# Kernel tuning notes

Hardware: AMD Instinct MI355X
Metric: run time of the kernel (lower is better)

## Reference

```python
import jax, jax.numpy as jnp
import numpy as np

T, HW, C = 64, 24, 1024
MID = 256
WIN = 2  # 'video' forward_type -> 2x2 windows


def setup_inputs() -> dict:
    key = jax.random.key(0)
    k1, k2, k3, k4, k5 = jax.random.split(key, 5)
    return {
        "image_features": jax.random.normal(k1, (T, HW * HW, C), dtype=jnp.float32),
        "Wq": jax.random.normal(k2, (C, MID), dtype=jnp.float32) * 0.02,
        "bq": jax.random.normal(k3, (MID,), dtype=jnp.float32) * 0.02,
        "Wk": jax.random.normal(k4, (C, MID), dtype=jnp.float32) * 0.02,
        "bk": jax.random.normal(k5, (MID,), dtype=jnp.float32) * 0.02,
    }


def reference(image_features, Wq, bq, Wk, bk):
    # forward_type == 'video': 2x2 windowed attention over pooled patches
    t, n, c = image_features.shape
    H = W = int(np.sqrt(n))
    h2, w2 = H // WIN, W // WIN
    # [T, H, W, C] -> [T, h2, 2, w2, 2, C] -> [T, h2, w2, 2, 2, C] -> [T, P, 4, C]
    x = image_features.reshape(t, h2, WIN, w2, WIN, c)
    windows = x.transpose(0, 1, 3, 2, 4, 5).reshape(t, h2 * w2, WIN * WIN, c)
    # avg_pool2d(2,2) == mean over each 2x2 window
    pooled = windows.mean(axis=2)  # [T, P, C]
    q = pooled @ Wq + bq           # [T, P, MID]
    k = windows @ Wk + bk          # [T, P, 4, MID]
    scale = 1.0 / jnp.sqrt(jnp.float32(MID))
    attn = jnp.einsum("tpd,tpwd->tpw", q, k) * scale  # [T, P, 4]
    attn = jnp.nan_to_num(attn)
    attn = jax.nn.softmax(attn, axis=-1)
    attn_feat = jnp.einsum("tpw,tpwc->tpc", attn, windows)  # softmax-weighted value avg
    # query dim has size 1, so .mean(1) in torch is identity here
    return pooled + attn_feat  # [T, P, C]; new_image_size = (h2, w2) is static
```

## Files before the change

kernel.cpp:

```cpp
#include <hip/hip_runtime.h>

#define T_ 64
#define P_ 144
#define NPAIR 9216
#define C_ 1024
#define MID_ 256

typedef __attribute__((ext_vector_type(4))) float f32x4;
typedef __attribute__((ext_vector_type(8))) __bf16 bf16x8;
typedef __attribute__((ext_vector_type(4))) __bf16 bf16x4;

__device__ __forceinline__ void async_copy16(const void* g, void* l) {
  __builtin_amdgcn_global_load_lds(
      (const __attribute__((address_space(1))) unsigned int*)g,
      (__attribute__((address_space(3))) unsigned int*)l, 16, 0, 0);
}

__device__ __forceinline__ void mfma_tile(const __bf16* As, const __bf16* Bs,
                                          int wm, int wn, int quad, int lr,
                                          f32x4 acc[4][4]) {
  bf16x8 a[4], b[4];
  const bf16x8* Ap = (const bf16x8*)As;
  const bf16x8* Bp = (const bf16x8*)Bs;
#pragma unroll
  for (int i = 0; i < 4; ++i) {
    a[i] = Ap[(wm * 64 + i * 16 + lr) * 4 + quad];
    b[i] = Bp[(wn * 64 + i * 16 + lr) * 4 + quad];
  }
#pragma unroll
  for (int mi = 0; mi < 4; ++mi)
#pragma unroll
    for (int ni = 0; ni < 4; ++ni)
      acc[mi][ni] = __builtin_amdgcn_mfma_f32_16x16x32_bf16(
          a[mi], b[ni], acc[mi][ni], 0, 0, 0);
}

__global__ __launch_bounds__(256) void prep_kernel(
    const float* __restrict__ img, const float* __restrict__ Wq,
    const float* __restrict__ bq, const float* __restrict__ Wk,
    __bf16* __restrict__ poolb, __bf16* __restrict__ H,
    float* __restrict__ kb) {
  __shared__ __align__(16) __bf16 As[128 * 32];
  __shared__ __align__(16) __bf16 Bs[128 * 32];
  const int bid = blockIdx.x;
  const int tid = threadIdx.x;
  if (bid < NPAIR) {
    const int t = bid / P_;
    const int p = bid - t * P_;
    const int wy = p / 12, wx = p - wy * 12;
    const int c = tid * 4;
    const float* base = img + ((size_t)t * 576 + 48 * wy + 2 * wx) * C_;
    f32x4 s = *(const f32x4*)(base + c);
    s += *(const f32x4*)(base + (size_t)1 * C_ + c);
    s += *(const f32x4*)(base + (size_t)24 * C_ + c);
    s += *(const f32x4*)(base + (size_t)25 * C_ + c);
    s *= 0.25f;
    bf16x4 pv;
#pragma unroll
    for (int j = 0; j < 4; ++j) pv[j] = (__bf16)s[j];
    *(bf16x4*)(poolb + (size_t)bid * C_ + c) = pv;
  } else if (bid < NPAIR + 64) {
    const int b = bid - NPAIR;
    const int mt = b >> 3, nt = b & 7;
    const int lane = tid & 63;
    const int wv = tid >> 6;
    const int quad = lane >> 4, lr = lane & 15;
    const int wm = wv >> 1, wn = wv & 1;
    const int r0 = tid >> 2, p0 = tid & 3;
    const float* ga0 = Wk + (size_t)(mt * 128 + r0) * MID_ + p0 * 8;
    const float* ga1 = ga0 + (size_t)64 * MID_;
    const float* gb0 = Wq + (size_t)(nt * 128 + r0) * MID_ + p0 * 8;
    const float* gb1 = gb0 + (size_t)64 * MID_;
    f32x4 acc[4][4] = {};
    for (int it = 0; it < 8; ++it) {
      const f32x4 a0 = *(const f32x4*)ga0, a1 = *(const f32x4*)(ga0 + 4);
      const f32x4 a2 = *(const f32x4*)ga1, a3 = *(const f32x4*)(ga1 + 4);
      const f32x4 b0 = *(const f32x4*)gb0, b1 = *(const f32x4*)(gb0 + 4);
      const f32x4 b2 = *(const f32x4*)gb1, b3 = *(const f32x4*)(gb1 + 4);
      ga0 += 32; ga1 += 32; gb0 += 32; gb1 += 32;
      bf16x8 ca0, ca1, cb0, cb1;
#pragma unroll
      for (int j = 0; j < 4; ++j) {
        ca0[j] = (__bf16)a0[j]; ca0[4 + j] = (__bf16)a1[j];
        ca1[j] = (__bf16)a2[j]; ca1[4 + j] = (__bf16)a3[j];
        cb0[j] = (__bf16)b0[j]; cb0[4 + j] = (__bf16)b1[j];
        cb1[j] = (__bf16)b2[j]; cb1[4 + j] = (__bf16)b3[j];
      }
      *(bf16x8*)(As + (size_t)tid * 8) = ca0;
      *(bf16x8*)(As + (size_t)(tid + 256) * 8) = ca1;
      *(bf16x8*)(Bs + (size_t)tid * 8) = cb0;
      *(bf16x8*)(Bs + (size_t)(tid + 256) * 8) = cb1;
      __syncthreads();
      mfma_tile(As, Bs, wm, wn, quad, lr, acc);
      __syncthreads();
    }
    const int colb = nt * 128 + wn * 64;
    const int rowb = mt * 128 + wm * 64 + quad * 4;
#pragma unroll
    for (int ni = 0; ni < 4; ++ni) {
      const int col = colb + ni * 16 + lr;
#pragma unroll
      for (int mi = 0; mi < 4; ++mi) {
        const int row = rowb + mi * 16;
#pragma unroll
        for (int r = 0; r < 4; ++r)
          H[(size_t)(row + r) * C_ + col] = (__bf16)acc[mi][ni][r];
      }
    }
  } else {
    __shared__ float bqs[256];
    bqs[tid] = bq[tid];
    __syncthreads();
    const int n = (bid - (NPAIR + 64)) * 256 + tid;
    const float* row = Wk + (size_t)n * MID_;
    float s = 0.f;
#pragma unroll 4
    for (int j = 0; j < 256; ++j) s += row[j] * bqs[j];
    kb[n] = s;
  }
}

__global__ __launch_bounds__(256) void gemm_u_kernel(
    const __bf16* __restrict__ A, const __bf16* __restrict__ Bt,
    const float* __restrict__ bias, __bf16* __restrict__ C) {
  __shared__ __align__(16) __bf16 As[128 * 32];
  __shared__ __align__(16) __bf16 Bs[128 * 32];
  const int bid = blockIdx.x;
  const int mt = bid >> 3, nt = bid & 7;
  const int tid = threadIdx.x;
  const int lane = tid & 63;
  const int wv = tid >> 6;
  const int quad = lane >> 4, lr = lane & 15;
  const int wm = wv >> 1, wn = wv & 1;

  const int r0 = tid >> 2, p0 = tid & 3;
  const int wvb = (tid & ~63) * 16;
  const __bf16* ga0 = A + ((size_t)mt * 128 + r0) * (size_t)C_ + p0 * 8;
  const __bf16* ga1 = ga0 + (size_t)64 * C_;
  const __bf16* gb0 = Bt + ((size_t)nt * 128 + r0) * (size_t)C_ + p0 * 8;
  const __bf16* gb1 = gb0 + (size_t)64 * C_;
  char* AsB0 = (char*)As + wvb;
  char* AsB1 = (char*)As + 4096 + wvb;
  char* BsB0 = (char*)Bs + wvb;
  char* BsB1 = (char*)Bs + 4096 + wvb;

  f32x4 acc[4][4] = {};

  for (int it = 0; it < 32; ++it) {
    async_copy16(ga0, AsB0);
    async_copy16(ga1, AsB1);
    async_copy16(gb0, BsB0);
    async_copy16(gb1, BsB1);
    ga0 += 32; ga1 += 32; gb0 += 32; gb1 += 32;
    __syncthreads();
    mfma_tile(As, Bs, wm, wn, quad, lr, acc);
    __syncthreads();
  }

  const int colb = nt * 128 + wn * 64;
  const int rowb = mt * 128 + wm * 64 + quad * 4;
#pragma unroll
  for (int ni = 0; ni < 4; ++ni) {
    const int col = colb + ni * 16 + lr;
    const float bv = bias[col];
#pragma unroll
    for (int mi = 0; mi < 4; ++mi) {
      const int row = rowb + mi * 16;
#pragma unroll
      for (int r = 0; r < 4; ++r)
        C[(size_t)(row + r) * C_ + col] = (__bf16)(acc[mi][ni][r] + bv);
    }
  }
}

__global__ void attn_out_kernel(const __bf16* __restrict__ U,
                                const float* __restrict__ img,
                                float* __restrict__ out) {
  const int pair = blockIdx.x;
  const int tid = threadIdx.x;
  const int wv = tid >> 6, lane = tid & 63;
  __shared__ float red[4][4];

  const int t = pair / P_;
  const int pp = pair - t * P_;
  const int wy = pp / 12, wx = pp - wy * 12;
  const float* base = img + ((size_t)t * 576 + 48 * wy + 2 * wx) * C_;
  const int c = tid * 4;
  f32x4 v0 = *(const f32x4*)(base + c);
  f32x4 v1 = *(const f32x4*)(base + (size_t)1 * C_ + c);
  f32x4 v2 = *(const f32x4*)(base + (size_t)24 * C_ + c);
  f32x4 v3 = *(const f32x4*)(base + (size_t)25 * C_ + c);
  const bf16x4 ub = *(const bf16x4*)(U + (size_t)pair * C_ + c);
  f32x4 u4;
#pragma unroll
  for (int j = 0; j < 4; ++j) u4[j] = (float)ub[j];

  float pd[4];
  pd[0] = u4[0] * v0[0] + u4[1] * v0[1] + u4[2] * v0[2] + u4[3] * v0[3];
  pd[1] = u4[0] * v1[0] + u4[1] * v1[1] + u4[2] * v1[2] + u4[3] * v1[3];
  pd[2] = u4[0] * v2[0] + u4[1] * v2[1] + u4[2] * v2[2] + u4[3] * v2[3];
  pd[3] = u4[0] * v3[0] + u4[1] * v3[1] + u4[2] * v3[2] + u4[3] * v3[3];

#pragma unroll
  for (int w = 0; w < 4; ++w) {
    float p = pd[w];
    p += __shfl_down(p, 32);
    p += __shfl_down(p, 16);
    p += __shfl_down(p, 8);
    p += __shfl_down(p, 4);
    p += __shfl_down(p, 2);
    p += __shfl_down(p, 1);
    if (lane == 0) red[w][wv] = p;
  }
  __syncthreads();
  float lg[4];
  float mx = -1e30f;
#pragma unroll
  for (int w = 0; w < 4; ++w) {
    lg[w] = (red[w][0] + red[w][1] + red[w][2] + red[w][3]) * 0.0625f;
    mx = fmaxf(mx, lg[w]);
  }
  float att[4];
  float ssum = 0.f;
#pragma unroll
  for (int w = 0; w < 4; ++w) {
    att[w] = __expf(lg[w] - mx);
    ssum += att[w];
  }
  const float inv = 1.f / ssum;
  const float a0 = att[0] * inv, a1 = att[1] * inv;
  const float a2 = att[2] * inv, a3 = att[3] * inv;

  f32x4 o = (v0 + v1 + v2 + v3) * 0.25f;
  o += a0 * v0 + a1 * v1 + a2 * v2 + a3 * v3;
  *(f32x4*)(out + (size_t)pair * C_ + c) = o;
}

extern "C" void kernel_launch(void* const* d_in, const int* in_sizes, int n_in,
                              void* d_out, int out_size, void* d_ws,
                              size_t ws_size, hipStream_t stream) {
  const float* img = (const float*)d_in[0];
  const float* Wq = (const float*)d_in[1];
  const float* bq = (const float*)d_in[2];
  const float* Wk = (const float*)d_in[3];
  const float* bk = (const float*)d_in[4];
  (void)bk;
  float* out = (float*)d_out;

  char* ws = (char*)d_ws;
  __bf16* poolb = (__bf16*)ws;
  __bf16* H = (__bf16*)(ws + 18874368);
  float* kb = (float*)(ws + 20971520);
  __bf16* U = (__bf16*)(ws + 20975616);

  prep_kernel<<<NPAIR + 68, 256, 0, stream>>>(img, Wq, bq, Wk, poolb, H, kb);
  gemm_u_kernel<<<576, 256, 0, stream>>>(poolb, H, kb, U);
  attn_out_kernel<<<NPAIR, 256, 0, stream>>>(U, img, out);
}
```

Baseline: 297.3 us.

## Fuse pooling, U GEMM and attention output into one per-16-window kernel

```diff
diff --git a/kernel.cpp b/kernel.cpp
--- a/kernel.cpp
+++ b/kernel.cpp
@@ -6,15 +6,13 @@
 #define C_ 1024
 #define MID_ 256
 
+#define MP 16
+#define PST 1032
+#define UST 1028
+
 typedef __attribute__((ext_vector_type(4))) float f32x4;
 typedef __attribute__((ext_vector_type(8))) __bf16 bf16x8;
 typedef __attribute__((ext_vector_type(4))) __bf16 bf16x4;
-
-__device__ __forceinline__ void async_copy16(const void* g, void* l) {
-  __builtin_amdgcn_global_load_lds(
-      (const __attribute__((address_space(1))) unsigned int*)g,
-      (__attribute__((address_space(3))) unsigned int*)l, 16, 0, 0);
-}
 
 __device__ __forceinline__ void mfma_tile(const __bf16* As, const __bf16* Bs,
                                           int wm, int wn, int quad, int lr,
@@ -36,32 +34,15 @@
 }
 
 __global__ __launch_bounds__(256) void prep_kernel(
-    const float* __restrict__ img, const float* __restrict__ Wq,
-    const float* __restrict__ bq, const float* __restrict__ Wk,
-    __bf16* __restrict__ poolb, __bf16* __restrict__ H,
+    const float* __restrict__ Wq, const float* __restrict__ bq,
+    const float* __restrict__ Wk, __bf16* __restrict__ H,
     float* __restrict__ kb) {
   __shared__ __align__(16) __bf16 As[128 * 32];
   __shared__ __align__(16) __bf16 Bs[128 * 32];
   const int bid = blockIdx.x;
   const int tid = threadIdx.x;
-  if (bid < NPAIR) {
-    const int t = bid / P_;
-    const int p = bid - t * P_;
-    const int wy = p / 12, wx = p - wy * 12;
-    const int c = tid * 4;
-    const float* base = img + ((size_t)t * 576 + 48 * wy + 2 * wx) * C_;
-    f32x4 s = *(const f32x4*)(base + c);
-    s += *(const f32x4*)(base + (size_t)1 * C_ + c);
-    s += *(const f32x4*)(base + (size_t)24 * C_ + c);
-    s += *(const f32x4*)(base + (size_t)25 * C_ + c);
-    s *= 0.25f;
-    bf16x4 pv;
-#pragma unroll
-    for (int j = 0; j < 4; ++j) pv[j] = (__bf16)s[j];
-    *(bf16x4*)(poolb + (size_t)bid * C_ + c) = pv;
-  } else if (bid < NPAIR + 64) {
-    const int b = bid - NPAIR;
-    const int mt = b >> 3, nt = b & 7;
+  if (bid < 64) {
+    const int mt = bid >> 3, nt = bid & 7;
     const int lane = tid & 63;
     const int wv = tid >> 6;
     const int quad = lane >> 4, lr = lane & 15;
@@ -111,7 +92,7 @@
     __shared__ float bqs[256];
     bqs[tid] = bq[tid];
     __syncthreads();
-    const int n = (bid - (NPAIR + 64)) * 256 + tid;
+    const int n = (bid - 64) * 256 + tid;
     const float* row = Wk + (size_t)n * MID_;
     float s = 0.f;
 #pragma unroll 4
@@ -120,120 +101,113 @@
   }
 }
 
-__global__ __launch_bounds__(256) void gemm_u_kernel(
-    const __bf16* __restrict__ A, const __bf16* __restrict__ Bt,
-    const float* __restrict__ bias, __bf16* __restrict__ C) {
-  __shared__ __align__(16) __bf16 As[128 * 32];
-  __shared__ __align__(16) __bf16 Bs[128 * 32];
+__global__ __launch_bounds__(512, 4) void fused_kernel(
+    const __bf16* __restrict__ H, const float* __restrict__ kb,
+    const float* __restrict__ img, float* __restrict__ out) {
+  __shared__ __align__(16) char ubuf[MP * UST * 4];
+  __shared__ float kbs[C_];
+  __bf16* pool_s = (__bf16*)ubuf;
+  float* u_s = (float*)ubuf;
+
+  const int tid = threadIdx.x;
   const int bid = blockIdx.x;
-  const int mt = bid >> 3, nt = bid & 7;
-  const int tid = threadIdx.x;
   const int lane = tid & 63;
   const int wv = tid >> 6;
   const int quad = lane >> 4, lr = lane & 15;
-  const int wm = wv >> 1, wn = wv & 1;
-
-  const int r0 = tid >> 2, p0 = tid & 3;
-  const int wvb = (tid & ~63) * 16;
-  const __bf16* ga0 = A + ((size_t)mt * 128 + r0) * (size_t)C_ + p0 * 8;
-  const __bf16* ga1 = ga0 + (size_t)64 * C_;
-  const __bf16* gb0 = Bt + ((size_t)nt * 128 + r0) * (size_t)C_ + p0 * 8;
-  const __bf16* gb1 = gb0 + (size_t)64 * C_;
-  char* AsB0 = (char*)As + wvb;
-  char* AsB1 = (char*)As + 4096 + wvb;
-  char* BsB0 = (char*)Bs + wvb;
-  char* BsB1 = (char*)Bs + 4096 + wvb;
-
-  f32x4 acc[4][4] = {};
-
-  for (int it = 0; it < 32; ++it) {
-    async_copy16(ga0, AsB0);
-    async_copy16(ga1, AsB1);
-    async_copy16(gb0, BsB0);
-    async_copy16(gb1, BsB1);
-    ga0 += 32; ga1 += 32; gb0 += 32; gb1 += 32;
-    __syncthreads();
-    mfma_tile(As, Bs, wm, wn, quad, lr, acc);
-    __syncthreads();
-  }
-
-  const int colb = nt * 128 + wn * 64;
-  const int rowb = mt * 128 + wm * 64 + quad * 4;
-#pragma unroll
-  for (int ni = 0; ni < 4; ++ni) {
-    const int col = colb + ni * 16 + lr;
-    const float bv = bias[col];
-#pragma unroll
-    for (int mi = 0; mi < 4; ++mi) {
-      const int row = rowb + mi * 16;
-#pragma unroll
-      for (int r = 0; r < 4; ++r)
-        C[(size_t)(row + r) * C_ + col] = (__bf16)(acc[mi][ni][r] + bv);
-    }
-  }
-}
-
-__global__ void attn_out_kernel(const __bf16* __restrict__ U,
-                                const float* __restrict__ img,
-                                float* __restrict__ out) {
-  const int pair = blockIdx.x;
-  const int tid = threadIdx.x;
-  const int wv = tid >> 6, lane = tid & 63;
-  __shared__ float red[4][4];
-
-  const int t = pair / P_;
-  const int pp = pair - t * P_;
+
+  const int p = tid >> 5;
+  const int lp = tid & 31;
+  const int gp = bid * MP + p;
+  const int t = gp / P_;
+  const int pp = gp - t * P_;
   const int wy = pp / 12, wx = pp - wy * 12;
   const float* base = img + ((size_t)t * 576 + 48 * wy + 2 * wx) * C_;
-  const int c = tid * 4;
-  f32x4 v0 = *(const f32x4*)(base + c);
-  f32x4 v1 = *(const f32x4*)(base + (size_t)1 * C_ + c);
-  f32x4 v2 = *(const f32x4*)(base + (size_t)24 * C_ + c);
-  f32x4 v3 = *(const f32x4*)(base + (size_t)25 * C_ + c);
-  const bf16x4 ub = *(const bf16x4*)(U + (size_t)pair * C_ + c);
-  f32x4 u4;
-#pragma unroll
-  for (int j = 0; j < 4; ++j) u4[j] = (float)ub[j];
-
-  float pd[4];
-  pd[0] = u4[0] * v0[0] + u4[1] * v0[1] + u4[2] * v0[2] + u4[3] * v0[3];
-  pd[1] = u4[0] * v1[0] + u4[1] * v1[1] + u4[2] * v1[2] + u4[3] * v1[3];
-  pd[2] = u4[0] * v2[0] + u4[1] * v2[1] + u4[2] * v2[2] + u4[3] * v2[3];
-  pd[3] = u4[0] * v3[0] + u4[1] * v3[1] + u4[2] * v3[2] + u4[3] * v3[3];
-
-#pragma unroll
-  for (int w = 0; w < 4; ++w) {
-    float p = pd[w];
-    p += __shfl_down(p, 32);
-    p += __shfl_down(p, 16);
-    p += __shfl_down(p, 8);
-    p += __shfl_down(p, 4);
-    p += __shfl_down(p, 2);
-    p += __shfl_down(p, 1);
-    if (lane == 0) red[w][wv] = p;
-  }
+
+#pragma unroll
+  for (int j = 0; j < 8; ++j) {
+    const int c = lp * 4 + j * 128;
+    f32x4 s = *(const f32x4*)(base + c);
+    s += *(const f32x4*)(base + C_ + c);
+    s += *(const f32x4*)(base + 24 * C_ + c);
+    s += *(const f32x4*)(base + 25 * C_ + c);
+    s *= 0.25f;
+    bf16x4 pv;
+#pragma unroll
+    for (int q = 0; q < 4; ++q) pv[q] = (__bf16)s[q];
+    *(bf16x4*)(pool_s + p * PST + c) = pv;
+  }
+  if (tid < 256) *(f32x4*)(kbs + tid * 4) = *(const f32x4*)(kb + tid * 4);
   __syncthreads();
-  float lg[4];
-  float mx = -1e30f;
-#pragma unroll
-  for (int w = 0; w < 4; ++w) {
-    lg[w] = (red[w][0] + red[w][1] + red[w][2] + red[w][3]) * 0.0625f;
-    mx = fmaxf(mx, lg[w]);
-  }
-  float att[4];
-  float ssum = 0.f;
-#pragma unroll
-  for (int w = 0; w < 4; ++w) {
-    att[w] = __expf(lg[w] - mx);
-    ssum += att[w];
-  }
-  const float inv = 1.f / ssum;
-  const float a0 = att[0] * inv, a1 = att[1] * inv;
-  const float a2 = att[2] * inv, a3 = att[3] * inv;
-
-  f32x4 o = (v0 + v1 + v2 + v3) * 0.25f;
-  o += a0 * v0 + a1 * v1 + a2 * v2 + a3 * v3;
-  *(f32x4*)(out + (size_t)pair * C_ + c) = o;
+
+  f32x4 acc[8] = {};
+  const __bf16* ap = pool_s + lr * PST + quad * 8;
+  const __bf16* hp[8];
+#pragma unroll
+  for (int j = 0; j < 8; ++j)
+    hp[j] = H + (size_t)(wv * 128 + j * 16 + lr) * C_ + quad * 8;
+  for (int it = 0; it < 32; ++it) {
+    const bf16x8 a = *(const bf16x8*)(ap + it * 32);
+    bf16x8 b[8];
+#pragma unroll
+    for (int j = 0; j < 8; ++j) b[j] = *(const bf16x8*)(hp[j] + it * 32);
+#pragma unroll
+    for (int j = 0; j < 8; ++j)
+      acc[j] = __builtin_amdgcn_mfma_f32_16x16x32_bf16(a, b[j], acc[j], 0, 0, 0);
+  }
+  __syncthreads();
+
+#pragma unroll
+  for (int j = 0; j < 8; ++j) {
+    const int col = wv * 128 + j * 16 + lr;
+    const float kv = kbs[col];
+#pragma unroll
+    for (int r = 0; r < 4; ++r)
+      u_s[(quad * 4 + r) * UST + col] = acc[j][r] + kv;
+  }
+  __syncthreads();
+
+  float pd0 = 0.f, pd1 = 0.f, pd2 = 0.f, pd3 = 0.f;
+  for (int j = 0; j < 8; ++j) {
+    const int c = lp * 4 + j * 128;
+    const f32x4 u4 = *(const f32x4*)(u_s + p * UST + c);
+    const f32x4 v0 = *(const f32x4*)(base + c);
+    const f32x4 v1 = *(const f32x4*)(base + C_ + c);
+    const f32x4 v2 = *(const f32x4*)(base + 24 * C_ + c);
+    const f32x4 v3 = *(const f32x4*)(base + 25 * C_ + c);
+#pragma unroll
+    for (int q = 0; q < 4; ++q) {
+      pd0 += u4[q] * v0[q];
+      pd1 += u4[q] * v1[q];
+      pd2 += u4[q] * v2[q];
+      pd3 += u4[q] * v3[q];
+    }
+  }
+#pragma unroll
+  for (int m = 16; m >= 1; m >>= 1) {
+    pd0 += __shfl_xor(pd0, m, 32);
+    pd1 += __shfl_xor(pd1, m, 32);
+    pd2 += __shfl_xor(pd2, m, 32);
+    pd3 += __shfl_xor(pd3, m, 32);
+  }
+  const float l0 = pd0 * 0.0625f, l1 = pd1 * 0.0625f;
+  const float l2 = pd2 * 0.0625f, l3 = pd3 * 0.0625f;
+  const float mx = fmaxf(fmaxf(l0, l1), fmaxf(l2, l3));
+  const float e0 = __expf(l0 - mx), e1 = __expf(l1 - mx);
+  const float e2 = __expf(l2 - mx), e3 = __expf(l3 - mx);
+  const float inv = 1.f / (e0 + e1 + e2 + e3);
+  const float a0 = e0 * inv, a1 = e1 * inv;
+  const float a2 = e2 * inv, a3 = e3 * inv;
+  float* op = out + (size_t)gp * C_;
+  for (int j = 0; j < 8; ++j) {
+    const int c = lp * 4 + j * 128;
+    const f32x4 v0 = *(const f32x4*)(base + c);
+    const f32x4 v1 = *(const f32x4*)(base + C_ + c);
+    const f32x4 v2 = *(const f32x4*)(base + 24 * C_ + c);
+    const f32x4 v3 = *(const f32x4*)(base + 25 * C_ + c);
+    f32x4 o = (v0 + v1 + v2 + v3) * 0.25f;
+    o += a0 * v0 + a1 * v1 + a2 * v2 + a3 * v3;
+    *(f32x4*)(op + c) = o;
+  }
 }
 
 extern "C" void kernel_launch(void* const* d_in, const int* in_sizes, int n_in,
@@ -248,12 +222,9 @@
   float* out = (float*)d_out;
 
   char* ws = (char*)d_ws;
-  __bf16* poolb = (__bf16*)ws;
-  __bf16* H = (__bf16*)(ws + 18874368);
-  float* kb = (float*)(ws + 20971520);
-  __bf16* U = (__bf16*)(ws + 20975616);
-
-  prep_kernel<<<NPAIR + 68, 256, 0, stream>>>(img, Wq, bq, Wk, poolb, H, kb);
-  gemm_u_kernel<<<576, 256, 0, stream>>>(poolb, H, kb, U);
-  attn_out_kernel<<<NPAIR, 256, 0, stream>>>(U, img, out);
-}
+  __bf16* H = (__bf16*)ws;
+  float* kb = (float*)(ws + 2097152);
+
+  prep_kernel<<<68, 256, 0, stream>>>(Wq, bq, Wk, H, kb);
+  fused_kernel<<<NPAIR / MP, 512, 0, stream>>>(H, kb, img, out);
+}
```

New measurement: 440.7 us. 1.48x slower.

## Fuse window pooling into the U GEMM, keeping pooled tiles in LDS

Applied to the files above, without the earlier changes.

```diff
diff --git a/kernel.cpp b/kernel.cpp
--- a/kernel.cpp
+++ b/kernel.cpp
@@ -5,6 +5,9 @@
 #define NPAIR 9216
 #define C_ 1024
 #define MID_ 256
+
+#define MP1 36
+#define PST 1032
 
 typedef __attribute__((ext_vector_type(4))) float f32x4;
 typedef __attribute__((ext_vector_type(8))) __bf16 bf16x8;
@@ -36,32 +39,15 @@
 }
 
 __global__ __launch_bounds__(256) void prep_kernel(
-    const float* __restrict__ img, const float* __restrict__ Wq,
-    const float* __restrict__ bq, const float* __restrict__ Wk,
-    __bf16* __restrict__ poolb, __bf16* __restrict__ H,
+    const float* __restrict__ Wq, const float* __restrict__ bq,
+    const float* __restrict__ Wk, __bf16* __restrict__ H,
     float* __restrict__ kb) {
   __shared__ __align__(16) __bf16 As[128 * 32];
   __shared__ __align__(16) __bf16 Bs[128 * 32];
   const int bid = blockIdx.x;
   const int tid = threadIdx.x;
-  if (bid < NPAIR) {
-    const int t = bid / P_;
-    const int p = bid - t * P_;
-    const int wy = p / 12, wx = p - wy * 12;
-    const int c = tid * 4;
-    const float* base = img + ((size_t)t * 576 + 48 * wy + 2 * wx) * C_;
-    f32x4 s = *(const f32x4*)(base + c);
-    s += *(const f32x4*)(base + (size_t)1 * C_ + c);
-    s += *(const f32x4*)(base + (size_t)24 * C_ + c);
-    s += *(const f32x4*)(base + (size_t)25 * C_ + c);
-    s *= 0.25f;
-    bf16x4 pv;
-#pragma unroll
-    for (int j = 0; j < 4; ++j) pv[j] = (__bf16)s[j];
-    *(bf16x4*)(poolb + (size_t)bid * C_ + c) = pv;
-  } else if (bid < NPAIR + 64) {
-    const int b = bid - NPAIR;
-    const int mt = b >> 3, nt = b & 7;
+  if (bid < 64) {
+    const int mt = bid >> 3, nt = bid & 7;
     const int lane = tid & 63;
     const int wv = tid >> 6;
     const int quad = lane >> 4, lr = lane & 15;
@@ -111,7 +97,7 @@
     __shared__ float bqs[256];
     bqs[tid] = bq[tid];
     __syncthreads();
-    const int n = (bid - (NPAIR + 64)) * 256 + tid;
+    const int n = (bid - 64) * 256 + tid;
     const float* row = Wk + (size_t)n * MID_;
     float s = 0.f;
 #pragma unroll 4
@@ -120,56 +106,86 @@
   }
 }
 
-__global__ __launch_bounds__(256) void gemm_u_kernel(
-    const __bf16* __restrict__ A, const __bf16* __restrict__ Bt,
-    const float* __restrict__ bias, __bf16* __restrict__ C) {
-  __shared__ __align__(16) __bf16 As[128 * 32];
-  __shared__ __align__(16) __bf16 Bs[128 * 32];
+__global__ __launch_bounds__(1024, 4) void pool_gemm_kernel(
+    const __bf16* __restrict__ H, const float* __restrict__ kb,
+    const float* __restrict__ img, __bf16* __restrict__ U) {
+  __shared__ __align__(16) __bf16 pool_s[MP1 * PST];
+  __shared__ __align__(16) __bf16 hs[1024 * 32];
+  __shared__ float kbs[C_];
+  const int tid = threadIdx.x;
   const int bid = blockIdx.x;
-  const int mt = bid >> 3, nt = bid & 7;
-  const int tid = threadIdx.x;
   const int lane = tid & 63;
   const int wv = tid >> 6;
   const int quad = lane >> 4, lr = lane & 15;
-  const int wm = wv >> 1, wn = wv & 1;
-
-  const int r0 = tid >> 2, p0 = tid & 3;
-  const int wvb = (tid & ~63) * 16;
-  const __bf16* ga0 = A + ((size_t)mt * 128 + r0) * (size_t)C_ + p0 * 8;
-  const __bf16* ga1 = ga0 + (size_t)64 * C_;
-  const __bf16* gb0 = Bt + ((size_t)nt * 128 + r0) * (size_t)C_ + p0 * 8;
-  const __bf16* gb1 = gb0 + (size_t)64 * C_;
-  char* AsB0 = (char*)As + wvb;
-  char* AsB1 = (char*)As + 4096 + wvb;
-  char* BsB0 = (char*)Bs + wvb;
-  char* BsB1 = (char*)Bs + 4096 + wvb;
-
-  f32x4 acc[4][4] = {};
+
+#pragma unroll
+  for (int s = 0; s < 9; ++s) {
+    const int cid = tid + s * 1024;
+    const int p = cid >> 8;
+    const int c = (cid & 255) * 4;
+    const int gp = bid * MP1 + p;
+    const int t = gp / P_;
+    const int pp = gp - t * P_;
+    const int wy = pp / 12, wx = pp - wy * 12;
+    const float* base = img + ((size_t)t * 576 + 48 * wy + 2 * wx) * C_;
+    f32x4 sm = *(const f32x4*)(base + c);
+    sm += *(const f32x4*)(base + C_ + c);
+    sm += *(const f32x4*)(base + 24 * C_ + c);
+    sm += *(const f32x4*)(base + 25 * C_ + c);
+    sm *= 0.25f;
+    bf16x4 pv;
+#pragma unroll
+    for (int q = 0; q < 4; ++q) pv[q] = (__bf16)sm[q];
+    *(bf16x4*)(pool_s + p * PST + c) = pv;
+  }
+  if (tid < 256) *(f32x4*)(kbs + tid * 4) = *(const f32x4*)(kb + tid * 4);
+
+  f32x4 acc[3][4] = {};
+  const int hrow = tid >> 2;
+  const __bf16* hsrc = H + (size_t)hrow * C_ + (tid & 3) * 8;
+  char* hdst = (char*)hs + tid * 16;
 
   for (int it = 0; it < 32; ++it) {
-    async_copy16(ga0, AsB0);
-    async_copy16(ga1, AsB1);
-    async_copy16(gb0, BsB0);
-    async_copy16(gb1, BsB1);
-    ga0 += 32; ga1 += 32; gb0 += 32; gb1 += 32;
+    const __bf16* src = hsrc + it * 32;
+#pragma unroll
+    for (int i = 0; i < 4; ++i)
+      async_copy16(src + (size_t)i * 256 * C_, hdst + i * 16384);
     __syncthreads();
-    mfma_tile(As, Bs, wm, wn, quad, lr, acc);
+    bf16x8 a[3], b[4];
+#pragma unroll
+    for (int mi = 0; mi < 3; ++mi)
+      a[mi] = *(const bf16x8*)(pool_s + (mi * 16 + lr) * PST + it * 32 + quad * 8);
+#pragma unroll
+    for (int j = 0; j < 4; ++j)
+      b[j] = *(const bf16x8*)(hs + (wv * 64 + j * 16 + lr) * 32 + quad * 8);
+#pragma unroll
+    for (int mi = 0; mi < 3; ++mi)
+#pragma unroll
+      for (int j = 0; j < 4; ++j)
+        acc[mi][j] = __builtin_amdgcn_mfma_f32_16x16x32_bf16(
+            a[mi], b[j], acc[mi][j], 0, 0, 0);
     __syncthreads();
   }
 
-  const int colb = nt * 128 + wn * 64;
-  const int rowb = mt * 128 + wm * 64 + quad * 4;
-#pragma unroll
-  for (int ni = 0; ni < 4; ++ni) {
-    const int col = colb + ni * 16 + lr;
-    const float bv = bias[col];
-#pragma unroll
-    for (int mi = 0; mi < 4; ++mi) {
-      const int row = rowb + mi * 16;
-#pragma unroll
-      for (int r = 0; r < 4; ++r)
-        C[(size_t)(row + r) * C_ + col] = (__bf16)(acc[mi][ni][r] + bv);
+#pragma unroll
+  for (int n = 0; n < 4; ++n) {
+    const int col = wv * 64 + n * 16 + lr;
+    const float kv = kbs[col];
+#pragma unroll
+    for (int mi = 0; mi < 3; ++mi) {
+      const int rowb = mi * 16 + quad * 4;
+#pragma unroll
+      for (int r = 0; r < 4; ++r) {
+        const int rr = rowb + r;
+        if (rr < MP1) pool_s[rr * PST + col] = (__bf16)(acc[mi][n][r] + kv);
+      }
     }
+  }
+  __syncthreads();
+  for (int i = tid; i < MP1 * 128; i += 1024) {
+    const int r = i >> 7, c8 = (i & 127) * 8;
+    *(bf16x8*)(U + ((size_t)bid * MP1 + r) * C_ + c8) =
+        *(const bf16x8*)(pool_s + r * PST + c8);
   }
 }
 
@@ -228,11 +244,10 @@
     ssum += att[w];
   }
   const float inv = 1.f / ssum;
-  const float a0 = att[0] * inv, a1 = att[1] * inv;
-  const float a2 = att[2] * inv, a3 = att[3] * inv;
-
-  f32x4 o = (v0 + v1 + v2 + v3) * 0.25f;
-  o += a0 * v0 + a1 * v1 + a2 * v2 + a3 * v3;
+  const float a0 = att[0] * inv + 0.25f, a1 = att[1] * inv + 0.25f;
+  const float a2 = att[2] * inv + 0.25f, a3 = att[3] * inv + 0.25f;
+
+  f32x4 o = a0 * v0 + a1 * v1 + a2 * v2 + a3 * v3;
   *(f32x4*)(out + (size_t)pair * C_ + c) = o;
 }
 
@@ -248,12 +263,11 @@
   float* out = (float*)d_out;
 
   char* ws = (char*)d_ws;
-  __bf16* poolb = (__bf16*)ws;
-  __bf16* H = (__bf16*)(ws + 18874368);
-  float* kb = (float*)(ws + 20971520);
-  __bf16* U = (__bf16*)(ws + 20975616);
-
-  prep_kernel<<<NPAIR + 68, 256, 0, stream>>>(img, Wq, bq, Wk, poolb, H, kb);
-  gemm_u_kernel<<<576, 256, 0, stream>>>(poolb, H, kb, U);
+  __bf16* H = (__bf16*)ws;
+  float* kb = (float*)(ws + 2097152);
+  __bf16* U = (__bf16*)(ws + 2101248);
+
+  prep_kernel<<<68, 256, 0, stream>>>(Wq, bq, Wk, H, kb);
+  pool_gemm_kernel<<<256, 1024, 0, stream>>>(H, kb, img, U);
   attn_out_kernel<<<NPAIR, 256, 0, stream>>>(U, img, out);
 }
```

Result: slower. 317.5 us (+6.8%).

## Reassociate projection to compute Q then Q·Wkᵀ instead of fused Wk·Wqᵀ matrix

Applied to the files above, without the earlier changes.

```diff
diff --git a/kernel.cpp b/kernel.cpp
--- a/kernel.cpp
+++ b/kernel.cpp
@@ -35,13 +35,10 @@
           a[mi], b[ni], acc[mi][ni], 0, 0, 0);
 }
 
-__global__ __launch_bounds__(256) void prep_kernel(
+__global__ __launch_bounds__(256) void pool_prep_kernel(
     const float* __restrict__ img, const float* __restrict__ Wq,
-    const float* __restrict__ bq, const float* __restrict__ Wk,
-    __bf16* __restrict__ poolb, __bf16* __restrict__ H,
-    float* __restrict__ kb) {
-  __shared__ __align__(16) __bf16 As[128 * 32];
-  __shared__ __align__(16) __bf16 Bs[128 * 32];
+    const float* __restrict__ Wk, __bf16* __restrict__ poolb,
+    __bf16* __restrict__ Wqt, __bf16* __restrict__ Wkb) {
   const int bid = blockIdx.x;
   const int tid = threadIdx.x;
   if (bid < NPAIR) {
@@ -61,72 +58,51 @@
     *(bf16x4*)(poolb + (size_t)bid * C_ + c) = pv;
   } else if (bid < NPAIR + 64) {
     const int b = bid - NPAIR;
-    const int mt = b >> 3, nt = b & 7;
-    const int lane = tid & 63;
-    const int wv = tid >> 6;
-    const int quad = lane >> 4, lr = lane & 15;
-    const int wm = wv >> 1, wn = wv & 1;
-    const int r0 = tid >> 2, p0 = tid & 3;
-    const float* ga0 = Wk + (size_t)(mt * 128 + r0) * MID_ + p0 * 8;
-    const float* ga1 = ga0 + (size_t)64 * MID_;
-    const float* gb0 = Wq + (size_t)(nt * 128 + r0) * MID_ + p0 * 8;
-    const float* gb1 = gb0 + (size_t)64 * MID_;
-    f32x4 acc[4][4] = {};
-    for (int it = 0; it < 8; ++it) {
-      const f32x4 a0 = *(const f32x4*)ga0, a1 = *(const f32x4*)(ga0 + 4);
-      const f32x4 a2 = *(const f32x4*)ga1, a3 = *(const f32x4*)(ga1 + 4);
-      const f32x4 b0 = *(const f32x4*)gb0, b1 = *(const f32x4*)(gb0 + 4);
-      const f32x4 b2 = *(const f32x4*)gb1, b3 = *(const f32x4*)(gb1 + 4);
-      ga0 += 32; ga1 += 32; gb0 += 32; gb1 += 32;
-      bf16x8 ca0, ca1, cb0, cb1;
-#pragma unroll
-      for (int j = 0; j < 4; ++j) {
-        ca0[j] = (__bf16)a0[j]; ca0[4 + j] = (__bf16)a1[j];
-        ca1[j] = (__bf16)a2[j]; ca1[4 + j] = (__bf16)a3[j];
-        cb0[j] = (__bf16)b0[j]; cb0[4 + j] = (__bf16)b1[j];
-        cb1[j] = (__bf16)b2[j]; cb1[4 + j] = (__bf16)b3[j];
-      }
-      *(bf16x8*)(As + (size_t)tid * 8) = ca0;
-      *(bf16x8*)(As + (size_t)(tid + 256) * 8) = ca1;
-      *(bf16x8*)(Bs + (size_t)tid * 8) = cb0;
-      *(bf16x8*)(Bs + (size_t)(tid + 256) * 8) = cb1;
-      __syncthreads();
-      mfma_tile(As, Bs, wm, wn, quad, lr, acc);
-      __syncthreads();
-    }
-    const int colb = nt * 128 + wn * 64;
-    const int rowb = mt * 128 + wm * 64 + quad * 4;
-#pragma unroll
-    for (int ni = 0; ni < 4; ++ni) {
-      const int col = colb + ni * 16 + lr;
-#pragma unroll
-      for (int mi = 0; mi < 4; ++mi) {
-        const int row = rowb + mi * 16;
-#pragma unroll
-        for (int r = 0; r < 4; ++r)
-          H[(size_t)(row + r) * C_ + col] = (__bf16)acc[mi][ni][r];
-      }
+    const int ct = b >> 3, dt = b & 7;
+    __shared__ float tile[128][33];
+    const int r = tid >> 3;
+    const int c4 = (tid & 7) * 4;
+#pragma unroll
+    for (int s = 0; s < 4; ++s) {
+      const int row = r + s * 32;
+      const f32x4 v =
+          *(const f32x4*)(Wq + (size_t)(ct * 128 + row) * MID_ + dt * 32 + c4);
+      tile[row][c4 + 0] = v[0]; tile[row][c4 + 1] = v[1];
+      tile[row][c4 + 2] = v[2]; tile[row][c4 + 3] = v[3];
+    }
+    __syncthreads();
+    const int dd = tid >> 5;
+    const int cc4 = (tid & 31) * 4;
+#pragma unroll
+    for (int s = 0; s < 4; ++s) {
+      const int d = dd + s * 8;
+      bf16x4 o;
+#pragma unroll
+      for (int j = 0; j < 4; ++j) o[j] = (__bf16)tile[cc4 + j][d];
+      *(bf16x4*)(Wqt + (size_t)(dt * 32 + d) * C_ + ct * 128 + cc4) = o;
     }
   } else {
-    __shared__ float bqs[256];
-    bqs[tid] = bq[tid];
-    __syncthreads();
-    const int n = (bid - (NPAIR + 64)) * 256 + tid;
-    const float* row = Wk + (size_t)n * MID_;
-    float s = 0.f;
-#pragma unroll 4
-    for (int j = 0; j < 256; ++j) s += row[j] * bqs[j];
-    kb[n] = s;
-  }
-}
-
-__global__ __launch_bounds__(256) void gemm_u_kernel(
+    const int b = bid - NPAIR - 64;
+    const float* src = Wk + (size_t)b * 8192;
+    __bf16* dst = Wkb + (size_t)b * 8192;
+#pragma unroll
+    for (int s = 0; s < 8; ++s) {
+      const f32x4 v = *(const f32x4*)(src + tid * 4 + s * 1024);
+      bf16x4 o;
+#pragma unroll
+      for (int j = 0; j < 4; ++j) o[j] = (__bf16)v[j];
+      *(bf16x4*)(dst + tid * 4 + s * 1024) = o;
+    }
+  }
+}
+
+__global__ __launch_bounds__(256) void gemm_q_kernel(
     const __bf16* __restrict__ A, const __bf16* __restrict__ Bt,
-    const float* __restrict__ bias, __bf16* __restrict__ C) {
+    const float* __restrict__ bias, __bf16* __restrict__ Q) {
   __shared__ __align__(16) __bf16 As[128 * 32];
   __shared__ __align__(16) __bf16 Bs[128 * 32];
   const int bid = blockIdx.x;
-  const int mt = bid >> 3, nt = bid & 7;
+  const int mt = bid >> 1, nt = bid & 1;
   const int tid = threadIdx.x;
   const int lane = tid & 63;
   const int wv = tid >> 6;
@@ -168,7 +144,59 @@
       const int row = rowb + mi * 16;
 #pragma unroll
       for (int r = 0; r < 4; ++r)
-        C[(size_t)(row + r) * C_ + col] = (__bf16)(acc[mi][ni][r] + bv);
+        Q[(size_t)(row + r) * MID_ + col] = (__bf16)(acc[mi][ni][r] + bv);
+    }
+  }
+}
+
+__global__ __launch_bounds__(256) void gemm_u_kernel(
+    const __bf16* __restrict__ A, const __bf16* __restrict__ Bt,
+    __bf16* __restrict__ U) {
+  __shared__ __align__(16) __bf16 As[128 * 32];
+  __shared__ __align__(16) __bf16 Bs[128 * 32];
+  const int bid = blockIdx.x;
+  const int mt = bid >> 3, nt = bid & 7;
+  const int tid = threadIdx.x;
+  const int lane = tid & 63;
+  const int wv = tid >> 6;
+  const int quad = lane >> 4, lr = lane & 15;
+  const int wm = wv >> 1, wn = wv & 1;
+
+  const int r0 = tid >> 2, p0 = tid & 3;
+  const int wvb = (tid & ~63) * 16;
+  const __bf16* ga0 = A + ((size_t)mt * 128 + r0) * (size_t)MID_ + p0 * 8;
+  const __bf16* ga1 = ga0 + (size_t)64 * MID_;
+  const __bf16* gb0 = Bt + ((size_t)nt * 128 + r0) * (size_t)MID_ + p0 * 8;
+  const __bf16* gb1 = gb0 + (size_t)64 * MID_;
+  char* AsB0 = (char*)As + wvb;
+  char* AsB1 = (char*)As + 4096 + wvb;
+  char* BsB0 = (char*)Bs + wvb;
+  char* BsB1 = (char*)Bs + 4096 + wvb;
+
+  f32x4 acc[4][4] = {};
+
+  for (int it = 0; it < 8; ++it) {
+    async_copy16(ga0, AsB0);
+    async_copy16(ga1, AsB1);
+    async_copy16(gb0, BsB0);
+    async_copy16(gb1, BsB1);
+    ga0 += 32; ga1 += 32; gb0 += 32; gb1 += 32;
+    __syncthreads();
+    mfma_tile(As, Bs, wm, wn, quad, lr, acc);
+    __syncthreads();
+  }
+
+  const int colb = nt * 128 + wn * 64;
+  const int rowb = mt * 128 + wm * 64 + quad * 4;
+#pragma unroll
+  for (int ni = 0; ni < 4; ++ni) {
+    const int col = colb + ni * 16 + lr;
+#pragma unroll
+    for (int mi = 0; mi < 4; ++mi) {
+      const int row = rowb + mi * 16;
+#pragma unroll
+      for (int r = 0; r < 4; ++r)
+        U[(size_t)(row + r) * C_ + col] = (__bf16)acc[mi][ni][r];
     }
   }
 }
@@ -228,11 +256,10 @@
     ssum += att[w];
   }
   const float inv = 1.f / ssum;
-  const float a0 = att[0] * inv, a1 = att[1] * inv;
-  const float a2 = att[2] * inv, a3 = att[3] * inv;
-
-  f32x4 o = (v0 + v1 + v2 + v3) * 0.25f;
-  o += a0 * v0 + a1 * v1 + a2 * v2 + a3 * v3;
+  const float a0 = att[0] * inv + 0.25f, a1 = att[1] * inv + 0.25f;
+  const float a2 = att[2] * inv + 0.25f, a3 = att[3] * inv + 0.25f;
+
+  f32x4 o = a0 * v0 + a1 * v1 + a2 * v2 + a3 * v3;
   *(f32x4*)(out + (size_t)pair * C_ + c) = o;
 }
 
@@ -249,11 +276,13 @@
 
   char* ws = (char*)d_ws;
   __bf16* poolb = (__bf16*)ws;
-  __bf16* H = (__bf16*)(ws + 18874368);
-  float* kb = (float*)(ws + 20971520);
-  __bf16* U = (__bf16*)(ws + 20975616);
-
-  prep_kernel<<<NPAIR + 68, 256, 0, stream>>>(img, Wq, bq, Wk, poolb, H, kb);
-  gemm_u_kernel<<<576, 256, 0, stream>>>(poolb, H, kb, U);
+  __bf16* Wqt = (__bf16*)(ws + 18874368);
+  __bf16* Wkb = (__bf16*)(ws + 19398656);
+  __bf16* Qb  = (__bf16*)(ws + 19922944);
+  __bf16* U   = (__bf16*)(ws + 24641536);
+
+  pool_prep_kernel<<<NPAIR + 96, 256, 0, stream>>>(img, Wq, Wk, poolb, Wqt, Wkb);
+  gemm_q_kernel<<<144, 256, 0, stream>>>(poolb, Wqt, bq, Qb);
+  gemm_u_kernel<<<576, 256, 0, stream>>>(Qb, Wkb, U);
   attn_out_kernel<<<NPAIR, 256, 0, stream>>>(U, img, out);
 }
```

Result: faster. 286.7 us (-3.6%).
